# Optimization experiments

Hardware: AMD Instinct MI355X
Metric: run time of the kernel (lower is better)

Reference implementation:

```python
import jax, jax.numpy as jnp
import numpy as np

T, B = 2048, 32
LIS, SPE, ATT = 1024, 1024, 512


def setup_inputs() -> dict:
    key = jax.random.key(0)
    ks = jax.random.split(key, 10)
    s = 0.02
    return {
        "listener_state": jax.random.normal(ks[0], (T, B, LIS), jnp.float32),
        "speller_state": jax.random.normal(ks[1], (B, SPE), jnp.float32),
        "listener_len": jax.random.randint(ks[2], (B,), 1, T + 1),
        "batch_size": B,
        "W_score": jax.random.normal(ks[3], (LIS, ATT), jnp.float32) * s,
        "b_score": jnp.zeros((ATT,), jnp.float32),
        "W_value": jax.random.normal(ks[4], (LIS, ATT), jnp.float32) * s,
        "b_value": jnp.zeros((ATT,), jnp.float32),
        "W_proj": jax.random.normal(ks[5], (SPE, ATT), jnp.float32) * s,
        "b_proj": jnp.zeros((ATT,), jnp.float32),
    }


def reference(listener_state, speller_state, listener_len, batch_size,
              W_score, b_score, W_value, b_value, W_proj, b_proj):
    # batch_first=False path: [T,B,D] -> [B,T,D]
    x = jnp.transpose(listener_state, (1, 0, 2))
    keys = jax.nn.relu(x @ W_score + b_score)          # [B,T,A]
    vals = jax.nn.relu(x @ W_value + b_value)          # [B,T,A]
    query = jax.nn.relu(speller_state @ W_proj + b_proj)  # [B,A]
    scores = jnp.einsum('ba,bta->bt', query, keys)     # [B,T]
    # vectorized length mask: additive -100 past valid length (faithful to source)
    t = jnp.arange(keys.shape[1])
    mask = jnp.where(t[None, :] >= listener_len[:, None], -100.0, 0.0)
    attn = jax.nn.softmax(scores + mask, axis=1)       # [B,T]
    context = jnp.einsum('bt,bta->ba', attn, vals)     # [B,A]
    return (context, attn)
```

## Files before the change

### kernel.cpp

```cpp
#include <hip/hip_runtime.h>
#include <hip/hip_bf16.h>
#include <hip/hip_fp16.h>

#define T_DIM 2048
#define B_DIM 32
#define LIS_DIM 1024
#define SPE_DIM 1024
#define ATT_DIM 512

typedef _Float16 f16x8 __attribute__((ext_vector_type(8)));
typedef _Float16 f16x4 __attribute__((ext_vector_type(4)));
typedef float f32x4 __attribute__((ext_vector_type(4)));

__global__ void transpose_w_kernel(const float* __restrict__ Ws,
                                   const float* __restrict__ Wv,
                                   _Float16* __restrict__ WTf) {
  __shared__ float t17[1024 * 17];
  int blk = blockIdx.x;
  int mat = blk >> 5, ct = blk & 31;
  int tid = threadIdx.x;
  const float* W = mat ? Wv : Ws;
  for (int e = tid; e < 16384; e += 256) {
    int k = e >> 4, c = e & 15;
    t17[k * 17 + c] = W[(size_t)k * ATT_DIM + ct * 16 + c];
  }
  __syncthreads();
  int wv4 = tid >> 6, lane = tid & 63, lo = lane & 15, hi = lane >> 4;
  for (int ks = wv4; ks < 32; ks += 4) {
    f16x8 h;
#pragma unroll
    for (int j = 0; j < 8; ++j)
      h[j] = (_Float16)t17[(ks * 32 + hi * 8 + j) * 17 + lo];
    ((f16x8*)WTf)[((size_t)((mat * 32 + ct) * 32 + ks)) * 64 + lane] = h;
  }
}

__global__ void query_kernel(const float* __restrict__ spe,
                             const float* __restrict__ Wp,
                             const float* __restrict__ bp,
                             float* __restrict__ q) {
  __shared__ float s[SPE_DIM];
  int b = blockIdx.x;
  for (int i = threadIdx.x; i < SPE_DIM; i += 256) s[i] = spe[(size_t)b * SPE_DIM + i];
  __syncthreads();
  for (int a = threadIdx.x; a < ATT_DIM; a += 256) {
    float acc = bp[a];
    for (int l = 0; l < SPE_DIM; ++l)
      acc = fmaf(s[l], Wp[(size_t)l * ATT_DIM + a], acc);
    q[(size_t)b * ATT_DIM + a] = fmaxf(acc, 0.f);
  }
}

__global__ __launch_bounds__(512, 2)
void dual_gemm_kernel(const float* __restrict__ x,
                      const _Float16* __restrict__ WTf,
                      const float* __restrict__ bs,
                      const float* __restrict__ bv,
                      const float* __restrict__ q,
                      float* __restrict__ scores,
                      _Float16* __restrict__ vals_p) {
  __shared__ __align__(16) char A_lds[2][16384];
  __shared__ float bk_s[ATT_DIM], bv_s[ATT_DIM], q_s[ATT_DIM];
  __shared__ float red_s[64];

  const int tid = threadIdx.x;
  const int blk = blockIdx.x;
  const int b = blk & 31;
  const int tc = blk >> 5;
  const int t0 = tc * 64;

  bk_s[tid] = bs[tid];
  bv_s[tid] = bv[tid];
  q_s[tid] = q[(size_t)b * ATT_DIM + tid];
  if (tid < 64) red_s[tid] = 0.f;

  const float* xb = x + (size_t)b * LIS_DIM;
  const int wv = tid >> 6;
  const int lane = tid & 63;
  const int lo = lane & 15;
  const int hi = lane >> 4;

  float4 sl[4];
  auto stage_load = [&](int c) {
    const int k0 = c * 128;
#pragma unroll
    for (int it = 0; it < 4; ++it) {
      int idx = it * 512 + tid;
      int row = idx >> 5;
      int c4 = idx & 31;
      sl[it] = ((const float4*)(xb + (size_t)(t0 + row) * (B_DIM * LIS_DIM) + k0))[c4];
    }
  };
  auto stage_write = [&](int c) {
    char* buf = A_lds[c & 1];
#pragma unroll
    for (int it = 0; it < 4; ++it) {
      int idx = it * 512 + tid;
      int row = idx >> 5;
      int c4 = idx & 31;
      f16x4 h;
      h[0] = (_Float16)sl[it].x; h[1] = (_Float16)sl[it].y;
      h[2] = (_Float16)sl[it].z; h[3] = (_Float16)sl[it].w;
      int off = (row * 256 + c4 * 8) ^ ((row & 7) << 4);
      *(f16x4*)(buf + off) = h;
    }
  };

  f32x4 kacc[4][4], vacc[4][4];
#pragma unroll
  for (int m = 0; m < 4; ++m)
#pragma unroll
    for (int n = 0; n < 4; ++n) {
      kacc[m][n] = (f32x4){0.f, 0.f, 0.f, 0.f};
      vacc[m][n] = (f32x4){0.f, 0.f, 0.f, 0.f};
    }

  stage_load(0);
  stage_write(0);
  __syncthreads();

  const f16x8* Wf = (const f16x8*)WTf;
  f16x8 wkf[2][4], wvf[2][4];
#pragma unroll
  for (int n = 0; n < 4; ++n) {
    wkf[0][n] = Wf[(size_t)((wv * 4 + n) * 32 + 0) * 64 + lane];
    wvf[0][n] = Wf[(size_t)((32 + wv * 4 + n) * 32 + 0) * 64 + lane];
  }

  for (int c = 0; c < 8; ++c) {
    if (c < 7) stage_load(c + 1);
    const char* buf = A_lds[c & 1];
#pragma unroll
    for (int kki = 0; kki < 4; ++kki) {
      const int ks = c * 4 + kki;
      const int kp = (ks + 1 < 32) ? ks + 1 : 31;
      const int cur = kki & 1, nxt = cur ^ 1;
#pragma unroll
      for (int n = 0; n < 4; ++n) {
        wkf[nxt][n] = Wf[(size_t)((wv * 4 + n) * 32 + kp) * 64 + lane];
        wvf[nxt][n] = Wf[(size_t)((32 + wv * 4 + n) * 32 + kp) * 64 + lane];
      }
      f16x8 bx[4];
#pragma unroll
      for (int m = 0; m < 4; ++m) {
        int row = m * 16 + lo;
        int off = (row * 256 + kki * 64 + hi * 16) ^ ((row & 7) << 4);
        bx[m] = *(const f16x8*)(buf + off);
      }
#pragma unroll
      for (int n = 0; n < 4; ++n)
#pragma unroll
        for (int m = 0; m < 4; ++m) {
          kacc[m][n] = __builtin_amdgcn_mfma_f32_16x16x32_f16(wkf[cur][n], bx[m], kacc[m][n], 0, 0, 0);
          vacc[m][n] = __builtin_amdgcn_mfma_f32_16x16x32_f16(wvf[cur][n], bx[m], vacc[m][n], 0, 0, 0);
        }
    }
    if (c < 7) stage_write(c + 1);
    __syncthreads();
  }

  _Float16* vp = vals_p + ((size_t)(b * 32 + tc) * 8 + wv) * 4096;
#pragma unroll
  for (int m = 0; m < 4; ++m)
#pragma unroll
    for (int n = 0; n < 4; ++n) {
      int col = wv * 64 + n * 16 + hi * 4;
      f16x4 h;
#pragma unroll
      for (int r = 0; r < 4; ++r)
        h[r] = (_Float16)fmaxf(vacc[m][n][r] + bv_s[col + r], 0.f);
      *(f16x4*)(vp + (m * 4 + n) * 256 + lane * 4) = h;
    }

  float sr[4] = {0.f, 0.f, 0.f, 0.f};
#pragma unroll
  for (int m = 0; m < 4; ++m)
#pragma unroll
    for (int n = 0; n < 4; ++n) {
      int col = wv * 64 + n * 16 + hi * 4;
#pragma unroll
      for (int r = 0; r < 4; ++r)
        sr[m] += q_s[col + r] * fmaxf(kacc[m][n][r] + bk_s[col + r], 0.f);
    }
#pragma unroll
  for (int m = 0; m < 4; ++m) {
    sr[m] += __shfl_xor(sr[m], 16, 64);
    sr[m] += __shfl_xor(sr[m], 32, 64);
    if (lane < 16) atomicAdd(&red_s[m * 16 + lo], sr[m]);
  }
  __syncthreads();
  if (tid < 64) scores[(size_t)b * T_DIM + t0 + tid] = red_s[tid];
}

__global__ void softmax_kernel(const float* __restrict__ scores,
                               const int* __restrict__ llen,
                               float* __restrict__ attn_out,
                               float* __restrict__ ctx_out) {
  __shared__ float rmax[4], rsum[4];
  int b = blockIdx.x, tid = threadIdx.x;
  int L = llen[b];
  float v[8];
  float mx = -1e30f;
  for (int i = 0; i < 8; ++i) {
    int t = i * 256 + tid;
    float s = scores[(size_t)b * T_DIM + t];
    if (t >= L) s -= 100.f;
    v[i] = s;
    mx = fmaxf(mx, s);
  }
  for (int d = 1; d < 64; d <<= 1) mx = fmaxf(mx, __shfl_xor(mx, d, 64));
  if ((tid & 63) == 0) rmax[tid >> 6] = mx;
  __syncthreads();
  mx = fmaxf(fmaxf(rmax[0], rmax[1]), fmaxf(rmax[2], rmax[3]));
  float sum = 0.f;
  for (int i = 0; i < 8; ++i) { v[i] = expf(v[i] - mx); sum += v[i]; }
  for (int d = 1; d < 64; d <<= 1) sum += __shfl_xor(sum, d, 64);
  if ((tid & 63) == 0) rsum[tid >> 6] = sum;
  __syncthreads();
  sum = rsum[0] + rsum[1] + rsum[2] + rsum[3];
  float inv = 1.f / sum;
  for (int i = 0; i < 8; ++i) {
    int t = i * 256 + tid;
    attn_out[(size_t)b * T_DIM + t] = v[i] * inv;
  }
  for (int i = tid; i < ATT_DIM; i += 256) ctx_out[(size_t)b * ATT_DIM + i] = 0.f;
}

__global__ __launch_bounds__(512)
void ctx_kernel(const _Float16* __restrict__ vals_p,
                const float* __restrict__ attn,
                float* __restrict__ ctx) {
  __shared__ float attn_s[512];
  int blk = blockIdx.x;
  int b = blk >> 2, tcg = blk & 3;
  int tid = threadIdx.x;
  int wv = tid >> 6, lane = tid & 63, lo = lane & 15, hi = lane >> 4;
  attn_s[tid] = attn[(size_t)b * T_DIM + tcg * 512 + tid];
  __syncthreads();
  float cacc[4][4] = {};
  for (int i = 0; i < 8; ++i) {
    int tc = tcg * 8 + i;
    const _Float16* vp = vals_p + ((size_t)(b * 32 + tc) * 8 + wv) * 4096;
#pragma unroll
    for (int m = 0; m < 4; ++m) {
      float w = attn_s[i * 64 + m * 16 + lo];
#pragma unroll
      for (int n = 0; n < 4; ++n) {
        f16x4 v = *(const f16x4*)(vp + (m * 4 + n) * 256 + lane * 4);
#pragma unroll
        for (int r = 0; r < 4; ++r) cacc[n][r] += w * (float)v[r];
      }
    }
  }
#pragma unroll
  for (int n = 0; n < 4; ++n)
#pragma unroll
    for (int r = 0; r < 4; ++r) {
      float v = cacc[n][r];
      v += __shfl_xor(v, 1, 64);
      v += __shfl_xor(v, 2, 64);
      v += __shfl_xor(v, 4, 64);
      v += __shfl_xor(v, 8, 64);
      if (lo == 0)
        atomicAdd(&ctx[(size_t)b * ATT_DIM + wv * 64 + n * 16 + hi * 4 + r], v);
    }
}

extern "C" void kernel_launch(void* const* d_in, const int* in_sizes, int n_in,
                              void* d_out, int out_size, void* d_ws, size_t ws_size,
                              hipStream_t stream) {
  const float* x   = (const float*)d_in[0];
  const float* spe = (const float*)d_in[1];
  const int*   len = (const int*)d_in[2];
  const float* Ws  = (const float*)d_in[4];
  const float* bs  = (const float*)d_in[5];
  const float* Wv  = (const float*)d_in[6];
  const float* bv  = (const float*)d_in[7];
  const float* Wp  = (const float*)d_in[8];
  const float* bp  = (const float*)d_in[9];
  float* out = (float*)d_out;

  char* ws = (char*)d_ws;
  _Float16* WTf  = (_Float16*)ws;
  float* q       = (float*)(ws + (2u << 20));
  float* scores  = (float*)(ws + (2u << 20) + (64u << 10));
  _Float16* vals = (_Float16*)(ws + (4u << 20));

  transpose_w_kernel<<<dim3(64), dim3(256), 0, stream>>>(Ws, Wv, WTf);
  query_kernel<<<dim3(32), dim3(256), 0, stream>>>(spe, Wp, bp, q);
  dual_gemm_kernel<<<dim3(1024), dim3(512), 0, stream>>>(x, WTf, bs, bv, q, scores, vals);
  softmax_kernel<<<dim3(32), dim3(256), 0, stream>>>(scores, len, out + 16384, out);
  ctx_kernel<<<dim3(128), dim3(512), 0, stream>>>(vals, out + 16384, out);
}
```

Before: 308.9 us.

## Retile GEMM into 256x256 blocks with LDS-staged weights and 32x32 MFMA

Splits the fused score/value GEMM into four column-block tiles of 256 rows by 256 columns, staging weights into shared memory via global_load_lds and using 32x32x16 MFMA with XCD-aware block swizzling. Scores accumulate across two column blocks via global atomics, with zeroing moved into a fused prep kernel that also performs weight transpose and query projection. The context kernel is rewritten for the new vals layout and writes results without atomics. This is meant to raise MFMA efficiency and weight reuse, at the cost of reading each x tile four times, relying on L2 hits.

After: 298.3 us. 3.4% less time.

```diff
diff --git a/kernel.cpp b/kernel.cpp
--- a/kernel.cpp
+++ b/kernel.cpp
@@ -11,191 +11,196 @@
 typedef _Float16 f16x8 __attribute__((ext_vector_type(8)));
 typedef _Float16 f16x4 __attribute__((ext_vector_type(4)));
 typedef float f32x4 __attribute__((ext_vector_type(4)));
-
-__global__ void transpose_w_kernel(const float* __restrict__ Ws,
-                                   const float* __restrict__ Wv,
-                                   _Float16* __restrict__ WTf) {
-  __shared__ float t17[1024 * 17];
-  int blk = blockIdx.x;
-  int mat = blk >> 5, ct = blk & 31;
-  int tid = threadIdx.x;
-  const float* W = mat ? Wv : Ws;
-  for (int e = tid; e < 16384; e += 256) {
-    int k = e >> 4, c = e & 15;
-    t17[k * 17 + c] = W[(size_t)k * ATT_DIM + ct * 16 + c];
-  }
-  __syncthreads();
-  int wv4 = tid >> 6, lane = tid & 63, lo = lane & 15, hi = lane >> 4;
-  for (int ks = wv4; ks < 32; ks += 4) {
-    f16x8 h;
-#pragma unroll
-    for (int j = 0; j < 8; ++j)
-      h[j] = (_Float16)t17[(ks * 32 + hi * 8 + j) * 17 + lo];
-    ((f16x8*)WTf)[((size_t)((mat * 32 + ct) * 32 + ks)) * 64 + lane] = h;
-  }
-}
-
-__global__ void query_kernel(const float* __restrict__ spe,
-                             const float* __restrict__ Wp,
-                             const float* __restrict__ bp,
-                             float* __restrict__ q) {
-  __shared__ float s[SPE_DIM];
-  int b = blockIdx.x;
-  for (int i = threadIdx.x; i < SPE_DIM; i += 256) s[i] = spe[(size_t)b * SPE_DIM + i];
-  __syncthreads();
-  for (int a = threadIdx.x; a < ATT_DIM; a += 256) {
-    float acc = bp[a];
-    for (int l = 0; l < SPE_DIM; ++l)
-      acc = fmaf(s[l], Wp[(size_t)l * ATT_DIM + a], acc);
-    q[(size_t)b * ATT_DIM + a] = fmaxf(acc, 0.f);
+typedef float f32x16 __attribute__((ext_vector_type(16)));
+typedef unsigned int u32;
+
+__global__ __launch_bounds__(256)
+void prep_kernel(const float* __restrict__ Ws, const float* __restrict__ Wv,
+                 _Float16* __restrict__ WTf, const float* __restrict__ spe,
+                 const float* __restrict__ Wp, const float* __restrict__ bp,
+                 float* __restrict__ q, float* __restrict__ scores) {
+  int p = blockIdx.x, tid = threadIdx.x;
+  if (p < 64) {
+    __shared__ float wlds[64 * 257];
+    int nb = p >> 4, c = p & 15;
+    const float* W = (nb >> 1) ? Wv : Ws;
+    int col0 = (nb & 1) * 256;
+    for (int i = 0; i < 64; ++i) {
+      int e = i * 256 + tid;
+      int r = e >> 8, cl = e & 255;
+      wlds[r * 257 + cl] = W[(size_t)(c * 64 + r) * ATT_DIM + col0 + cl];
+    }
+    __syncthreads();
+    int lane = tid & 63, ks = tid >> 6, hk = lane >> 5, cs = lane & 31;
+#pragma unroll
+    for (int ct = 0; ct < 8; ++ct) {
+      f16x8 h;
+#pragma unroll
+      for (int jj = 0; jj < 8; ++jj)
+        h[jj] = (_Float16)wlds[(ks * 16 + hk * 8 + jj) * 257 + ct * 32 + cs];
+      ((f16x8*)WTf)[(size_t)(((p * 4 + ks) * 8 + ct)) * 64 + lane] = h;
+    }
+  } else if (p < 96) {
+    __shared__ float s[SPE_DIM];
+    int b = p - 64;
+    for (int i = tid; i < SPE_DIM; i += 256) s[i] = spe[(size_t)b * SPE_DIM + i];
+    __syncthreads();
+    for (int a = tid; a < ATT_DIM; a += 256) {
+      float acc = bp[a];
+      for (int l = 0; l < SPE_DIM; ++l)
+        acc = fmaf(s[l], Wp[(size_t)l * ATT_DIM + a], acc);
+      q[(size_t)b * ATT_DIM + a] = fmaxf(acc, 0.f);
+    }
+  } else {
+    int base = (p - 96) * 8192;
+    for (int i = 0; i < 32; ++i) scores[base + i * 256 + tid] = 0.f;
   }
 }
 
 __global__ __launch_bounds__(512, 2)
-void dual_gemm_kernel(const float* __restrict__ x,
-                      const _Float16* __restrict__ WTf,
-                      const float* __restrict__ bs,
-                      const float* __restrict__ bv,
-                      const float* __restrict__ q,
-                      float* __restrict__ scores,
-                      _Float16* __restrict__ vals_p) {
-  __shared__ __align__(16) char A_lds[2][16384];
-  __shared__ float bk_s[ATT_DIM], bv_s[ATT_DIM], q_s[ATT_DIM];
-  __shared__ float red_s[64];
+void gemm_kernel(const float* __restrict__ x, const _Float16* __restrict__ WTf,
+                 const float* __restrict__ bs, const float* __restrict__ bv,
+                 const float* __restrict__ q, float* __restrict__ scores,
+                 _Float16* __restrict__ vals_p) {
+  __shared__ __align__(16) _Float16 A_lds[2][16384];
+  __shared__ __align__(16) _Float16 W_lds[2][16384];
+  __shared__ float bias_s[256], q_s[256], red_s[256];
 
   const int tid = threadIdx.x;
-  const int blk = blockIdx.x;
-  const int b = blk & 31;
-  const int tc = blk >> 5;
-  const int t0 = tc * 64;
-
-  bk_s[tid] = bs[tid];
-  bv_s[tid] = bv[tid];
-  q_s[tid] = q[(size_t)b * ATT_DIM + tid];
-  if (tid < 64) red_s[tid] = 0.f;
+  const int raw = blockIdx.x;
+  const int xcd = raw & 7;
+  const int j   = raw >> 3;
+  const int nb  = j & 3;
+  const int tile = (j >> 2) * 8 + xcd;
+  const int b   = tile >> 3;
+  const int tm  = tile & 7;
+  const int t0  = tm * 256;
+  const bool is_scores = (nb < 2);
+
+  const float* bias_src = is_scores ? (bs + (nb & 1) * 256) : (bv + (nb & 1) * 256);
+  if (tid < 256) {
+    bias_s[tid] = bias_src[tid];
+    red_s[tid] = 0.f;
+    if (is_scores) q_s[tid] = q[(size_t)b * ATT_DIM + nb * 256 + tid];
+  }
+
+  const int wv = tid >> 6, lane = tid & 63;
+  const int wr = wv >> 2, wc = wv & 3;
+  const int ts = lane & 31, hk = lane >> 5;
 
   const float* xb = x + (size_t)b * LIS_DIM;
-  const int wv = tid >> 6;
-  const int lane = tid & 63;
-  const int lo = lane & 15;
-  const int hi = lane >> 4;
-
-  float4 sl[4];
+  f32x4 sl[8];
   auto stage_load = [&](int c) {
-    const int k0 = c * 128;
-#pragma unroll
-    for (int it = 0; it < 4; ++it) {
-      int idx = it * 512 + tid;
-      int row = idx >> 5;
-      int c4 = idx & 31;
-      sl[it] = ((const float4*)(xb + (size_t)(t0 + row) * (B_DIM * LIS_DIM) + k0))[c4];
+#pragma unroll
+    for (int i = 0; i < 8; ++i) {
+      int e = i * 512 + tid;
+      int row = e >> 4, q4 = e & 15;
+      sl[i] = *((const f32x4*)(xb + (size_t)(t0 + row) * (B_DIM * LIS_DIM) + c * 64) + q4);
     }
   };
-  auto stage_write = [&](int c) {
-    char* buf = A_lds[c & 1];
-#pragma unroll
-    for (int it = 0; it < 4; ++it) {
-      int idx = it * 512 + tid;
-      int row = idx >> 5;
-      int c4 = idx & 31;
+  auto stage_write = [&](int bufi) {
+    char* buf = (char*)A_lds[bufi];
+#pragma unroll
+    for (int i = 0; i < 8; ++i) {
+      int e = i * 512 + tid;
+      int row = e >> 4, q4 = e & 15;
       f16x4 h;
-      h[0] = (_Float16)sl[it].x; h[1] = (_Float16)sl[it].y;
-      h[2] = (_Float16)sl[it].z; h[3] = (_Float16)sl[it].w;
-      int off = (row * 256 + c4 * 8) ^ ((row & 7) << 4);
-      *(f16x4*)(buf + off) = h;
+      h[0] = (_Float16)sl[i][0]; h[1] = (_Float16)sl[i][1];
+      h[2] = (_Float16)sl[i][2]; h[3] = (_Float16)sl[i][3];
+      *(f16x4*)(buf + row * 128 + ((q4 * 8) ^ ((row & 7) << 4))) = h;
     }
   };
-
-  f32x4 kacc[4][4], vacc[4][4];
+  auto w_prefetch = [&](int c, int bufi) {
+    const char* slice = (const char*)WTf + ((size_t)(nb * 16 + c)) * 32768;
+    char* lb = (char*)W_lds[bufi] + wv * 1024;
+#pragma unroll
+    for (int i = 0; i < 4; ++i) {
+      __builtin_amdgcn_global_load_lds(
+          (const __attribute__((address_space(1))) u32*)(slice + i * 8192 + tid * 16),
+          (__attribute__((address_space(3))) u32*)(lb + i * 8192), 16, 0, 0);
+    }
+  };
+
+  f32x16 acc[4][2];
 #pragma unroll
   for (int m = 0; m < 4; ++m)
 #pragma unroll
-    for (int n = 0; n < 4; ++n) {
-      kacc[m][n] = (f32x4){0.f, 0.f, 0.f, 0.f};
-      vacc[m][n] = (f32x4){0.f, 0.f, 0.f, 0.f};
-    }
-
+    for (int n = 0; n < 2; ++n)
+      acc[m][n] = (f32x16)(0.f);
+
+  w_prefetch(0, 0);
   stage_load(0);
   stage_write(0);
-  __syncthreads();
-
-  const f16x8* Wf = (const f16x8*)WTf;
-  f16x8 wkf[2][4], wvf[2][4];
-#pragma unroll
-  for (int n = 0; n < 4; ++n) {
-    wkf[0][n] = Wf[(size_t)((wv * 4 + n) * 32 + 0) * 64 + lane];
-    wvf[0][n] = Wf[(size_t)((32 + wv * 4 + n) * 32 + 0) * 64 + lane];
-  }
-
-  for (int c = 0; c < 8; ++c) {
-    if (c < 7) stage_load(c + 1);
-    const char* buf = A_lds[c & 1];
-#pragma unroll
-    for (int kki = 0; kki < 4; ++kki) {
-      const int ks = c * 4 + kki;
-      const int kp = (ks + 1 < 32) ? ks + 1 : 31;
-      const int cur = kki & 1, nxt = cur ^ 1;
-#pragma unroll
-      for (int n = 0; n < 4; ++n) {
-        wkf[nxt][n] = Wf[(size_t)((wv * 4 + n) * 32 + kp) * 64 + lane];
-        wvf[nxt][n] = Wf[(size_t)((32 + wv * 4 + n) * 32 + kp) * 64 + lane];
+  asm volatile("s_waitcnt vmcnt(0) lgkmcnt(0)" ::: "memory");
+  __builtin_amdgcn_s_barrier();
+
+  for (int c = 0; c < 16; ++c) {
+    const int bi = c & 1;
+    if (c < 15) { w_prefetch(c + 1, bi ^ 1); stage_load(c + 1); }
+    const char* Ab = (const char*)A_lds[bi];
+    const char* Wb = (const char*)W_lds[bi];
+#pragma unroll
+    for (int ks = 0; ks < 4; ++ks) {
+      f16x8 wf[2], bx[4];
+#pragma unroll
+      for (int n = 0; n < 2; ++n)
+        wf[n] = *(const f16x8*)(Wb + (ks * 8 + wc * 2 + n) * 1024 + lane * 16);
+#pragma unroll
+      for (int m = 0; m < 4; ++m) {
+        int row = wr * 128 + m * 32 + ts;
+        bx[m] = *(const f16x8*)(Ab + row * 128 + ((ks * 32 + hk * 16) ^ ((row & 7) << 4)));
       }
-      f16x8 bx[4];
-#pragma unroll
-      for (int m = 0; m < 4; ++m) {
-        int row = m * 16 + lo;
-        int off = (row * 256 + kki * 64 + hi * 16) ^ ((row & 7) << 4);
-        bx[m] = *(const f16x8*)(buf + off);
-      }
-#pragma unroll
-      for (int n = 0; n < 4; ++n)
-#pragma unroll
-        for (int m = 0; m < 4; ++m) {
-          kacc[m][n] = __builtin_amdgcn_mfma_f32_16x16x32_f16(wkf[cur][n], bx[m], kacc[m][n], 0, 0, 0);
-          vacc[m][n] = __builtin_amdgcn_mfma_f32_16x16x32_f16(wvf[cur][n], bx[m], vacc[m][n], 0, 0, 0);
+      __builtin_amdgcn_s_setprio(1);
+#pragma unroll
+      for (int n = 0; n < 2; ++n)
+#pragma unroll
+        for (int m = 0; m < 4; ++m)
+          acc[m][n] = __builtin_amdgcn_mfma_f32_32x32x16_f16(wf[n], bx[m], acc[m][n], 0, 0, 0);
+      __builtin_amdgcn_s_setprio(0);
+    }
+    if (c < 15) stage_write(bi ^ 1);
+    asm volatile("s_waitcnt vmcnt(0) lgkmcnt(0)" ::: "memory");
+    __builtin_amdgcn_s_barrier();
+  }
+
+  if (is_scores) {
+#pragma unroll
+    for (int m = 0; m < 4; ++m) {
+      float s = 0.f;
+#pragma unroll
+      for (int n = 0; n < 2; ++n)
+#pragma unroll
+        for (int rg = 0; rg < 16; ++rg) {
+          int cl = wc * 64 + n * 32 + (rg & 3) + 8 * (rg >> 2) + 4 * hk;
+          s += q_s[cl] * fmaxf(acc[m][n][rg] + bias_s[cl], 0.f);
         }
-    }
-    if (c < 7) stage_write(c + 1);
+      s += __shfl_xor(s, 32, 64);
+      if (lane < 32) atomicAdd(&red_s[wr * 128 + m * 32 + ts], s);
+    }
     __syncthreads();
-  }
-
-  _Float16* vp = vals_p + ((size_t)(b * 32 + tc) * 8 + wv) * 4096;
-#pragma unroll
-  for (int m = 0; m < 4; ++m)
-#pragma unroll
-    for (int n = 0; n < 4; ++n) {
-      int col = wv * 64 + n * 16 + hi * 4;
-      f16x4 h;
-#pragma unroll
-      for (int r = 0; r < 4; ++r)
-        h[r] = (_Float16)fmaxf(vacc[m][n][r] + bv_s[col + r], 0.f);
-      *(f16x4*)(vp + (m * 4 + n) * 256 + lane * 4) = h;
-    }
-
-  float sr[4] = {0.f, 0.f, 0.f, 0.f};
-#pragma unroll
-  for (int m = 0; m < 4; ++m)
-#pragma unroll
-    for (int n = 0; n < 4; ++n) {
-      int col = wv * 64 + n * 16 + hi * 4;
-#pragma unroll
-      for (int r = 0; r < 4; ++r)
-        sr[m] += q_s[col + r] * fmaxf(kacc[m][n][r] + bk_s[col + r], 0.f);
-    }
-#pragma unroll
-  for (int m = 0; m < 4; ++m) {
-    sr[m] += __shfl_xor(sr[m], 16, 64);
-    sr[m] += __shfl_xor(sr[m], 32, 64);
-    if (lane < 16) atomicAdd(&red_s[m * 16 + lo], sr[m]);
-  }
-  __syncthreads();
-  if (tid < 64) scores[(size_t)b * T_DIM + t0 + tid] = red_s[tid];
+    if (tid < 256) atomicAdd(&scores[(size_t)b * T_DIM + t0 + tid], red_s[tid]);
+  } else {
+    _Float16* vb = vals_p + (((size_t)tile * 2 + (nb - 2)) * 8 + wv) * 8192;
+#pragma unroll
+    for (int m = 0; m < 4; ++m)
+#pragma unroll
+      for (int n = 0; n < 2; ++n)
+#pragma unroll
+        for (int g = 0; g < 4; ++g) {
+          f16x4 h;
+#pragma unroll
+          for (int r = 0; r < 4; ++r) {
+            int cl = wc * 64 + n * 32 + 8 * g + 4 * hk + r;
+            h[r] = (_Float16)fmaxf(acc[m][n][g * 4 + r] + bias_s[cl], 0.f);
+          }
+          *(f16x4*)(vb + (size_t)(((m * 2 + n) * 4 + g) * 64 + lane) * 4) = h;
+        }
+  }
 }
 
 __global__ void softmax_kernel(const float* __restrict__ scores,
                                const int* __restrict__ llen,
-                               float* __restrict__ attn_out,
-                               float* __restrict__ ctx_out) {
+                               float* __restrict__ attn_out) {
   __shared__ float rmax[4], rsum[4];
   int b = blockIdx.x, tid = threadIdx.x;
   int L = llen[b];
@@ -219,50 +224,54 @@
   __syncthreads();
   sum = rsum[0] + rsum[1] + rsum[2] + rsum[3];
   float inv = 1.f / sum;
-  for (int i = 0; i < 8; ++i) {
-    int t = i * 256 + tid;
-    attn_out[(size_t)b * T_DIM + t] = v[i] * inv;
-  }
-  for (int i = tid; i < ATT_DIM; i += 256) ctx_out[(size_t)b * ATT_DIM + i] = 0.f;
+  for (int i = 0; i < 8; ++i)
+    attn_out[(size_t)b * T_DIM + i * 256 + tid] = v[i] * inv;
 }
 
 __global__ __launch_bounds__(512)
 void ctx_kernel(const _Float16* __restrict__ vals_p,
                 const float* __restrict__ attn,
                 float* __restrict__ ctx) {
-  __shared__ float attn_s[512];
+  __shared__ float attn_s[T_DIM];
   int blk = blockIdx.x;
-  int b = blk >> 2, tcg = blk & 3;
+  int b = blk >> 1, nb2 = blk & 1;
   int tid = threadIdx.x;
-  int wv = tid >> 6, lane = tid & 63, lo = lane & 15, hi = lane >> 4;
-  attn_s[tid] = attn[(size_t)b * T_DIM + tcg * 512 + tid];
+#pragma unroll
+  for (int i = 0; i < 4; ++i)
+    attn_s[i * 512 + tid] = attn[(size_t)b * T_DIM + i * 512 + tid];
   __syncthreads();
-  float cacc[4][4] = {};
-  for (int i = 0; i < 8; ++i) {
-    int tc = tcg * 8 + i;
-    const _Float16* vp = vals_p + ((size_t)(b * 32 + tc) * 8 + wv) * 4096;
-#pragma unroll
-    for (int m = 0; m < 4; ++m) {
-      float w = attn_s[i * 64 + m * 16 + lo];
-#pragma unroll
-      for (int n = 0; n < 4; ++n) {
-        f16x4 v = *(const f16x4*)(vp + (m * 4 + n) * 256 + lane * 4);
-#pragma unroll
-        for (int r = 0; r < 4; ++r) cacc[n][r] += w * (float)v[r];
+  int w = tid >> 6, L = tid & 63;
+  int wc = w >> 1, n = w & 1, h = L >> 5, ts = L & 31;
+  float acc[4][4] = {};
+  for (int tm = 0; tm < 8; ++tm) {
+    int tile = b * 8 + tm;
+#pragma unroll
+    for (int wr = 0; wr < 2; ++wr) {
+      const _Float16* base = vals_p + (((size_t)tile * 2 + nb2) * 8 + (wr * 4 + wc)) * 8192;
+#pragma unroll
+      for (int m = 0; m < 4; ++m) {
+        float a = attn_s[tm * 256 + wr * 128 + m * 32 + ts];
+#pragma unroll
+        for (int g = 0; g < 4; ++g) {
+          f16x4 v = *(const f16x4*)(base + (size_t)(((m * 2 + n) * 4 + g) * 64 + L) * 4);
+#pragma unroll
+          for (int r = 0; r < 4; ++r) acc[g][r] += a * (float)v[r];
+        }
       }
     }
   }
 #pragma unroll
-  for (int n = 0; n < 4; ++n)
+  for (int g = 0; g < 4; ++g)
 #pragma unroll
     for (int r = 0; r < 4; ++r) {
-      float v = cacc[n][r];
-      v += __shfl_xor(v, 1, 64);
-      v += __shfl_xor(v, 2, 64);
-      v += __shfl_xor(v, 4, 64);
-      v += __shfl_xor(v, 8, 64);
-      if (lo == 0)
-        atomicAdd(&ctx[(size_t)b * ATT_DIM + wv * 64 + n * 16 + hi * 4 + r], v);
+      float v2 = acc[g][r];
+      v2 += __shfl_xor(v2, 1, 64);
+      v2 += __shfl_xor(v2, 2, 64);
+      v2 += __shfl_xor(v2, 4, 64);
+      v2 += __shfl_xor(v2, 8, 64);
+      v2 += __shfl_xor(v2, 16, 64);
+      if (ts == 0)
+        ctx[(size_t)b * ATT_DIM + nb2 * 256 + wc * 64 + n * 32 + 8 * g + 4 * h + r] = v2;
     }
 }
 
@@ -286,9 +295,8 @@
   float* scores  = (float*)(ws + (2u << 20) + (64u << 10));
   _Float16* vals = (_Float16*)(ws + (4u << 20));
 
-  transpose_w_kernel<<<dim3(64), dim3(256), 0, stream>>>(Ws, Wv, WTf);
-  query_kernel<<<dim3(32), dim3(256), 0, stream>>>(spe, Wp, bp, q);
-  dual_gemm_kernel<<<dim3(1024), dim3(512), 0, stream>>>(x, WTf, bs, bv, q, scores, vals);
-  softmax_kernel<<<dim3(32), dim3(256), 0, stream>>>(scores, len, out + 16384, out);
-  ctx_kernel<<<dim3(128), dim3(512), 0, stream>>>(vals, out + 16384, out);
-}
+  prep_kernel<<<dim3(104), dim3(256), 0, stream>>>(Ws, Wv, WTf, spe, Wp, bp, q, scores);
+  gemm_kernel<<<dim3(1024), dim3(512), 0, stream>>>(x, WTf, bs, bv, q, scores, vals);
+  softmax_kernel<<<dim3(32), dim3(256), 0, stream>>>(scores, len, out + 16384);
+  ctx_kernel<<<dim3(64), dim3(512), 0, stream>>>(vals, out + 16384, out);
+}
```
